# Kernel tuning notes

Measured on AMD Instinct MI355X. Metric: run time of the kernel, lower is better.

The kernel has to match this reference:

```python
import jax, jax.numpy as jnp
import numpy as np

N = 20000      # nodes
E = 80000      # edges (before self loops)
NG = 64        # graphs in batch
EMB = 780      # embedding_size (768 text + 12 time)
NEG_SLOPE = 0.2
BN_EPS = 1e-5


def setup_inputs() -> dict:
    key = jax.random.key(0)
    ks = jax.random.split(key, 20)
    def rn(k, shape, s=0.05):
        return jax.random.normal(k, shape, dtype=jnp.float32) * s
    z = lambda n: jnp.zeros((n,), dtype=jnp.float32)
    o = lambda n: jnp.ones((n,), dtype=jnp.float32)
    x = jax.random.normal(ks[0], (N, 772), dtype=jnp.float32)
    edge_index = jax.random.randint(ks[1], (2, E), 0, N)
    batch = jnp.sort(jax.random.randint(ks[2], (N,), 0, NG))
    return dict(
        x=x, edge_index=edge_index, batch=batch,
        time_W=rn(ks[3], (4, 12)), time_b=z(12),
        lin_W0=rn(ks[4], (EMB, 3 * EMB)), att_src0=rn(ks[5], (3, EMB)), att_dst0=rn(ks[6], (3, EMB)),
        bias0=z(3 * EMB), gamma0=o(3 * EMB), beta0=z(3 * EMB),
        lin_W1=rn(ks[7], (3 * EMB, 3 * EMB)), att_src1=rn(ks[8], (3, EMB)), att_dst1=rn(ks[9], (3, EMB)),
        bias1=z(3 * EMB), gamma1=o(3 * EMB), beta1=z(3 * EMB),
        lin_W2=rn(ks[10], (3 * EMB, EMB)), att_src2=rn(ks[11], (1, EMB)), att_dst2=rn(ks[12], (1, EMB)),
        bias2=z(EMB), gamma2=o(EMB), beta2=z(EMB),
        mlp_W1=rn(ks[13], (EMB, 128)), mlp_b1=z(128),
        mlp_W2=rn(ks[14], (128, 64)), mlp_b2=z(64),
    )


def _gat_layer(h, src, dst, W, a_src, a_dst, b, heads):
    # PyG GATConv (eval mode: dropout off), concat=True, self loops already in src/dst
    C = W.shape[1] // heads
    hp = (h @ W).reshape(N, heads, C)                       # [N,H,C]
    a_s = jnp.sum(hp * a_src[None], axis=-1)                # [N,H]
    a_d = jnp.sum(hp * a_dst[None], axis=-1)                # [N,H]
    e = jax.nn.leaky_relu(a_s[src] + a_d[dst], NEG_SLOPE)   # [E+N,H]
    m = jax.ops.segment_max(e, dst, num_segments=N)         # segment softmax over incoming edges
    m = jnp.where(jnp.isfinite(m), m, 0.0)
    p = jnp.exp(e - m[dst])
    denom = jax.ops.segment_sum(p, dst, num_segments=N)
    alpha = p / (denom[dst] + 1e-16)                        # [E+N,H]
    out = jax.ops.segment_sum(alpha[:, :, None] * hp[src], dst, num_segments=N)  # [N,H,C]
    return out.reshape(N, heads * C) + b


def _bn(h, gamma, beta):
    # BatchNorm in training-mode math (batch statistics, biased variance)
    mu = jnp.mean(h, axis=0)
    var = jnp.mean((h - mu) ** 2, axis=0)
    return (h - mu) * jax.lax.rsqrt(var + BN_EPS) * gamma + beta


def reference(x, edge_index, batch, time_W, time_b,
              lin_W0, att_src0, att_dst0, bias0, gamma0, beta0,
              lin_W1, att_src1, att_dst1, bias1, gamma1, beta1,
              lin_W2, att_src2, att_dst2, bias2, gamma2, beta2,
              mlp_W1, mlp_b1, mlp_W2, mlp_b2):
    te = x[:, 768:772] @ time_W + time_b
    h = jnp.concatenate([jax.lax.stop_gradient(x[:, :768]), te,
                         jax.lax.stop_gradient(x[:, 772:])], axis=-1)  # [N, 780]
    sl = jnp.arange(N)
    src = jnp.concatenate([edge_index[0], sl])   # add self loops
    dst = jnp.concatenate([edge_index[1], sl])
    layers = [
        (lin_W0, att_src0, att_dst0, bias0, gamma0, beta0, 3),
        (lin_W1, att_src1, att_dst1, bias1, gamma1, beta1, 3),
        (lin_W2, att_src2, att_dst2, bias2, gamma2, beta2, 1),
    ]
    for W, a_s, a_d, b, g, bt, heads in layers:
        h = jnp.tanh(_gat_layer(h, src, dst, W, a_s, a_d, b, heads))
        h = _bn(h, g, bt)
    cnt = jax.ops.segment_sum(jnp.ones((N,), dtype=h.dtype), batch, num_segments=NG)
    pooled = jax.ops.segment_sum(h, batch, num_segments=NG) / jnp.maximum(cnt, 1.0)[:, None]
    pooled = jax.nn.relu(pooled)
    out = jnp.tanh(pooled @ mlp_W1 + mlp_b1) @ mlp_W2 + mlp_b2
    return out  # [NG, 64]
```

## Files before the change

kernel.cpp:

```cpp
#include <hip/hip_runtime.h>
#include <math.h>

#define NN   20000
#define EE   80000
#define ELP  100000
#define NGR  64
#define EMB  780
#define W3   2340
#define EMBP 832
#define W3P  2368
#define NZ   (W3+8)

static inline int cdiv_i(long long a, long long b){ return (int)((a + b - 1) / b); }

typedef _Float16 f16;
typedef _Float16 f16x4 __attribute__((ext_vector_type(4)));
typedef _Float16 f16x8 __attribute__((ext_vector_type(8)));
typedef float    f32x4 __attribute__((ext_vector_type(4)));

__device__ __forceinline__ void async_ld16(const f16* g, f16* l){
    __builtin_amdgcn_global_load_lds(
        (const __attribute__((address_space(1))) unsigned int*)g,
        (__attribute__((address_space(3))) unsigned int*)l,
        16, 0, 0);
}

__global__ void k_zero_f32(float* p, int n){
    int i = blockIdx.x*256 + threadIdx.x; if (i < n) p[i] = 0.f;
}
__global__ void k_zero_i32(int* p, int n){
    int i = blockIdx.x*256 + threadIdx.x; if (i < n) p[i] = 0;
}

__global__ void k_transpose(const float* __restrict__ W, f16* __restrict__ Wt,
                            const float* __restrict__ sc, const float* __restrict__ sh,
                            float* __restrict__ dvec, int K, int N, int KP){
    __shared__ float T[32][33];
    __shared__ float D[8][33];
    int n0 = blockIdx.x*32, k0 = blockIdx.y*32;
    int tx = threadIdx.x, ty = threadIdx.y;
    float raw[4];
#pragma unroll
    for (int r = 0; r < 4; r++){
        int k = k0 + ty + r*8;
        float w = 0.f;
        if (k < K && n0 + tx < N) w = W[(size_t)k*N + n0 + tx];
        raw[r] = w;
        T[ty + r*8][tx] = sc ? w * ((k < K) ? sc[k] : 0.f) : w;
    }
    if (sh){
        float p = 0.f;
#pragma unroll
        for (int r = 0; r < 4; r++){
            int k = k0 + ty + r*8;
            if (k < K) p += sh[k] * raw[r];
        }
        D[ty][tx] = p;
    }
    __syncthreads();
#pragma unroll
    for (int r = 0; r < 4; r++){
        int n = n0 + ty + r*8;
        int k = k0 + tx;
        if (n < N && k < KP) Wt[(size_t)n*KP + k] = (f16)T[tx][ty + r*8];
    }
    if (sh && ty == 0 && n0 + tx < N){
        float s = 0.f;
#pragma unroll
        for (int j = 0; j < 8; j++) s += D[j][tx];
        atomicAdd(&dvec[n0 + tx], s);
    }
}

__global__ void k_wvec(const float* __restrict__ W, const float* __restrict__ asrc,
                       const float* __restrict__ adst, const float* __restrict__ sc,
                       f16* __restrict__ Wt, float* __restrict__ dvec,
                       int K, int N, int KP, int H){
    int k = blockIdx.x*4 + (threadIdx.x >> 6);
    int lane = threadIdx.x & 63;
    if (k < K){
        const float* row = W + (size_t)k*N;
        float acc[6];
#pragma unroll
        for (int i = 0; i < 6; i++) acc[i] = 0.f;
        for (int c = lane; c < EMB; c += 64){
            for (int h = 0; h < H; h++){
                float wv = row[h*EMB + c];
                acc[h]     += wv * asrc[h*EMB + c];
                acc[H + h] += wv * adst[h*EMB + c];
            }
        }
        float s = sc ? sc[k] : 1.f;
        for (int i = 0; i < 2*H; i++){
            float v = acc[i];
#pragma unroll
            for (int off = 32; off; off >>= 1) v += __shfl_xor(v, off);
            if (lane == 0) Wt[(size_t)(N + i)*KP + k] = (f16)(v * s);
        }
    }
    if (blockIdx.x == 0){
        int wv = threadIdx.x >> 6;
        for (int i = wv; i < 2*H; i += 4){
            int h = (i < H) ? i : (i - H);
            const float* att = (i < H) ? (asrc + h*EMB) : (adst + h*EMB);
            float s = 0.f;
            for (int c = lane; c < EMB; c += 64) s += dvec[h*EMB + c] * att[c];
#pragma unroll
            for (int off = 32; off; off >>= 1) s += __shfl_xor(s, off);
            if (lane == 0) dvec[N + i] = s;
        }
    }
}

__global__ void k_build_h(const float* __restrict__ x, const float* __restrict__ tW,
                          const float* __restrict__ tb, f16* __restrict__ h){
    int idx = blockIdx.x*256 + threadIdx.x;
    int total = NN*(EMBP/4);
    if (idx >= total) return;
    int n = idx / (EMBP/4);
    int c0 = (idx - n*(EMBP/4))*4;
    const float* xr = x + (size_t)n*772;
    f16x4 o;
#pragma unroll
    for (int j = 0; j < 4; j++){
        int c = c0 + j; float v;
        if (c < 768) v = xr[c];
        else if (c < EMB){
            int t = c - 768;
            v = tb[t] + xr[768]*tW[t] + xr[769]*tW[12+t] + xr[770]*tW[24+t] + xr[771]*tW[36+t];
        } else v = 0.f;
        o[j] = (f16)v;
    }
    *(f16x4*)(h + (size_t)n*EMBP + c0) = o;
}

__global__ void k_deg(const int* __restrict__ ei, int* __restrict__ deg){
    int k = blockIdx.x*256 + threadIdx.x; if (k >= ELP) return;
    int d = (k < EE) ? ei[EE + k] : (k - EE);
    atomicAdd(&deg[d], 1);
}

__global__ __launch_bounds__(1024) void k_scan(int* __restrict__ deg, int* __restrict__ rp){
    __shared__ int part[1024];
    int tid = threadIdx.x;
    int i0 = tid*20;
    int n = (i0 < NN) ? min(20, NN - i0) : 0;
    int s = 0;
    for (int k = 0; k < n; k++) s += deg[i0+k];
    part[tid] = s; __syncthreads();
    for (int off = 1; off < 1024; off <<= 1){
        int t = (tid >= off) ? part[tid-off] : 0;
        __syncthreads();
        part[tid] += t;
        __syncthreads();
    }
    int run = part[tid] - s;
    for (int k = 0; k < n; k++){
        int d = deg[i0+k];
        rp[i0+k] = run;
        deg[i0+k] = run;
        run += d;
    }
    if (tid == 1023) rp[NN] = part[1023];
}

__global__ void k_fill(const int* __restrict__ ei, int* __restrict__ cursor, int* __restrict__ csrc){
    int k = blockIdx.x*256 + threadIdx.x; if (k >= ELP) return;
    int s, d;
    if (k < EE){ s = ei[k]; d = ei[EE + k]; } else { s = k - EE; d = s; }
    int pos = atomicAdd(&cursor[d], 1);
    csrc[pos] = s;
}

__global__ void k_grp(const int* __restrict__ batch, int* __restrict__ grp){
    int g = blockIdx.x*256 + threadIdx.x; if (g > NGR) return;
    int lo = 0, hi = NN;
    while (lo < hi){ int mid = (lo+hi)>>1; if (batch[mid] < g) lo = mid+1; else hi = mid; }
    grp[g] = lo;
}

__global__ __launch_bounds__(256) void k_gemm_mfma(const f16* __restrict__ A,
                                                   const f16* __restrict__ Bt,
                                                   const float* __restrict__ dvec,
                                                   f16* __restrict__ C,
                                                   float* __restrict__ a_sd,
                                                   int M, int N, int NB, int H,
                                                   int KP, int SN,
                                                   int Mtiles, int NT){
    int bid = blockIdx.x;
    int xcd = bid & 7;
    int j   = bid >> 3;
    int sl  = j / NT;
    int nt  = j - sl*NT;
    int mt  = sl*8 + xcd;
    if (mt >= Mtiles) return;
    int m0 = mt*128, n0 = nt*128;

    __shared__ f16 smem[128*136];
    f16* As = smem;
    f16* Bs = smem + 8192;
    int tid = threadIdx.x;
    int w = tid >> 6, lane = tid & 63;

    int lrow = lane >> 2;
    int lko  = (lane & 3) * 8;

    int i2a = w*2, i2b = w*2 + 1;
    const f16* gA0 = A  + (size_t)min(m0 + i2a*16 + lrow, M-1)*KP + lko;
    const f16* gA1 = A  + (size_t)min(m0 + i2b*16 + lrow, M-1)*KP + lko;
    const f16* gB0 = Bt + (size_t)min(n0 + i2a*16 + lrow, NB-1)*KP + lko;
    const f16* gB1 = Bt + (size_t)min(n0 + i2b*16 + lrow, NB-1)*KP + lko;
    f16* lA0 = &As[i2a*512]; f16* lA1 = &As[i2b*512];
    f16* lB0 = &Bs[i2a*512]; f16* lB1 = &Bs[i2b*512];

    f32x4 acc[4][4];
#pragma unroll
    for (int i = 0; i < 4; i++)
#pragma unroll
        for (int j2 = 0; j2 < 4; j2++) acc[i][j2] = (f32x4)0.f;

    int wm = (w & 1) * 64, wn = (w >> 1) * 64;
    int lq = lane >> 4, lm = lane & 15;

    for (int kk = 0; kk < KP; kk += 64){
        __syncthreads();
        async_ld16(gA0 + kk, lA0);
        async_ld16(gA1 + kk, lA1);
        async_ld16(gB0 + kk, lB0);
        async_ld16(gB1 + kk, lB1);
        async_ld16(gA0 + kk + 32, lA0 + 4096);
        async_ld16(gA1 + kk + 32, lA1 + 4096);
        async_ld16(gB0 + kk + 32, lB0 + 4096);
        async_ld16(gB1 + kk + 32, lB1 + 4096);
        __syncthreads();

#pragma unroll
        for (int half = 0; half < 2; half++){
            const f16* Ap = As + half*4096;
            const f16* Bp = Bs + half*4096;
            f16x8 aF[4], bF[4];
#pragma unroll
            for (int mi = 0; mi < 4; mi++)
                aF[mi] = *(const f16x8*)&Ap[(wm + mi*16 + lm)*32 + lq*8];
#pragma unroll
            for (int ni = 0; ni < 4; ni++)
                bF[ni] = *(const f16x8*)&Bp[(wn + ni*16 + lm)*32 + lq*8];
#pragma unroll
            for (int mi = 0; mi < 4; mi++)
#pragma unroll
                for (int ni = 0; ni < 4; ni++)
                    acc[mi][ni] = __builtin_amdgcn_mfma_f32_16x16x32_f16(aF[mi], bF[ni], acc[mi][ni], 0, 0, 0);
        }
    }

#pragma unroll
    for (int mi = 0; mi < 4; mi++){
#pragma unroll
        for (int ni = 0; ni < 4; ni++){
            int col = n0 + wn + ni*16 + lm;
            if (col >= N && col < NB){
                int jc = col - N;
                int idx = (jc < H) ? jc : (3 + jc - H);
                float dv = dvec[col];
                int rbase = m0 + wm + mi*16 + lq*4;
#pragma unroll
                for (int r = 0; r < 4; r++){
                    int row = rbase + r;
                    if (row < M) a_sd[(size_t)row*6 + idx] = acc[mi][ni][r] + dv;
                }
            }
        }
    }

    if (n0 < N){
        __syncthreads();
#pragma unroll
        for (int mi = 0; mi < 4; mi++){
#pragma unroll
            for (int ni = 0; ni < 4; ni++){
                int col = wn + ni*16 + lm;
                int gcol = n0 + col;
                float dv = (gcol < N) ? dvec[gcol] : 0.f;
#pragma unroll
                for (int r = 0; r < 4; r++){
                    int row = wm + mi*16 + lq*4 + r;
                    smem[row*136 + col] = (f16)(acc[mi][ni][r] + dv);
                }
            }
        }
        __syncthreads();
        int ncols = min(128, N - n0);
#pragma unroll
        for (int it = 0; it < 8; it++){
            int ch = tid + it*256;
            int row = ch >> 4, cc = (ch & 15)*8;
            int grow = m0 + row;
            if (grow < M && cc < ncols){
                if (cc + 8 <= ncols){
                    f16x8 v = *(f16x8*)&smem[row*136 + cc];
                    *(f16x8*)(C + (size_t)grow*SN + n0 + cc) = v;
                } else {
                    for (int jj = cc; jj < ncols; jj++)
                        C[(size_t)grow*SN + n0 + jj] = smem[row*136 + jj];
                }
            }
        }
    }
}

template<int H>
__global__ __launch_bounds__(256) void k_agg2(const f16* __restrict__ hp, const int* __restrict__ rp,
                                              const int* __restrict__ csrc, const float* __restrict__ a_sd,
                                              const float* __restrict__ bias,
                                              f16* __restrict__ y, int SP, int W){
    int n = blockIdx.x, tid = threadIdx.x, lane = tid & 63;
    int beg = rp[n], deg = rp[n+1] - beg;

    float adv[H];
#pragma unroll
    for (int h = 0; h < H; h++) adv[h] = a_sd[(size_t)n*6 + 3 + h];

    float mx[H];
#pragma unroll
    for (int h = 0; h < H; h++) mx[h] = -1e30f;
    for (int base = 0; base < deg; base += 64){
        int e = base + lane;
        if (e < deg){
            int s = csrc[beg + e];
#pragma unroll
            for (int h = 0; h < H; h++){
                float t = a_sd[(size_t)s*6 + h] + adv[h];
                t = t > 0.f ? t : 0.2f*t;
                mx[h] = fmaxf(mx[h], t);
            }
        }
    }
#pragma unroll
    for (int off = 32; off; off >>= 1)
#pragma unroll
        for (int h = 0; h < H; h++) mx[h] = fmaxf(mx[h], __shfl_xor(mx[h], off));

    float dn[H];
#pragma unroll
    for (int h = 0; h < H; h++) dn[h] = 0.f;
    for (int base = 0; base < deg; base += 64){
        int e = base + lane;
        if (e < deg){
            int s = csrc[beg + e];
#pragma unroll
            for (int h = 0; h < H; h++){
                float t = a_sd[(size_t)s*6 + h] + adv[h];
                t = t > 0.f ? t : 0.2f*t;
                dn[h] += expf(t - mx[h]);
            }
        }
    }
#pragma unroll
    for (int off = 32; off; off >>= 1)
#pragma unroll
        for (int h = 0; h < H; h++) dn[h] += __shfl_xor(dn[h], off);
    float inv[H];
#pragma unroll
    for (int h = 0; h < H; h++) inv[h] = 1.f / (dn[h] + 1e-16f);

    float acc[2][8];
#pragma unroll
    for (int g = 0; g < 2; g++)
#pragma unroll
        for (int j = 0; j < 8; j++) acc[g][j] = 0.f;
    int  cg[2];  cg[0] = tid*8; cg[1] = 2048 + tid*8;
    bool act[2]; act[0] = cg[0] < W; act[1] = cg[1] < W;
    int hlo[2], hhi[2], nsp[2];
#pragma unroll
    for (int g = 0; g < 2; g++){
        int c = cg[g];
        int hl = min(c / EMB, H-1);
        int hh = min((c+7) / EMB, H-1);
        hlo[g] = hl; hhi[g] = hh;
        nsp[g] = (hh > hl) ? (EMB*(hl+1) - c) : 8;
    }

    for (int base = 0; base < deg; base += 64){
        int cnt = min(64, deg - base);
        int sl = 0; float al[H];
        {
            int e = base + lane;
            if (e < deg){
                sl = csrc[beg + e];
#pragma unroll
                for (int h = 0; h < H; h++){
                    float t = a_sd[(size_t)sl*6 + h] + adv[h];
                    t = t > 0.f ? t : 0.2f*t;
                    al[h] = expf(t - mx[h]) * inv[h];
                }
            } else {
#pragma unroll
                for (int h = 0; h < H; h++) al[h] = 0.f;
            }
        }
#pragma unroll 4
        for (int e = 0; e < cnt; e++){
            int s = __shfl(sl, e);
            float a0 = __shfl(al[0], e);
            float a1 = (H==3) ? __shfl(al[1], e) : a0;
            float a2 = (H==3) ? __shfl(al[2], e) : a0;
            const f16* row = hp + (size_t)s*SP;
#pragma unroll
            for (int g = 0; g < 2; g++){
                if (act[g]){
                    f16x8 v = *(const f16x8*)(row + cg[g]);
                    float lo = (hlo[g]==0) ? a0 : (hlo[g]==1 ? a1 : a2);
                    float hi = (hhi[g]==0) ? a0 : (hhi[g]==1 ? a1 : a2);
#pragma unroll
                    for (int j = 0; j < 8; j++){
                        float alj = (j < nsp[g]) ? lo : hi;
                        acc[g][j] += alj * (float)v[j];
                    }
                }
            }
        }
    }

#pragma unroll
    for (int g = 0; g < 2; g++){
        int c = cg[g];
        if (c < SP){
            f16x8 o;
#pragma unroll
            for (int j = 0; j < 8; j++){
                float vv = (c + j < W) ? tanhf(acc[g][j] + bias[c+j]) : 0.f;
                o[j] = (f16)vv;
            }
            *(f16x8*)(y + (size_t)n*SP + c) = o;
        }
    }
}

__global__ void k_bnstat(const f16* __restrict__ y, float* __restrict__ ps,
                         float* __restrict__ pq, int W, int SP){
    int c0 = (blockIdx.x*256 + threadIdx.x)*4;
    if (c0 >= W) return;
    int slice = blockIdx.y;
    int r0 = (int)(((long long)NN*slice)/128);
    int r1 = (int)(((long long)NN*(slice+1))/128);
    float s[4] = {0,0,0,0}, q[4] = {0,0,0,0};
    for (int r = r0; r < r1; r++){
        f16x4 u = *(const f16x4*)(y + (size_t)r*SP + c0);
#pragma unroll
        for (int j = 0; j < 4; j++){ float v = (float)u[j]; s[j] += v; q[j] += v*v; }
    }
#pragma unroll
    for (int j = 0; j < 4; j++){
        ps[(size_t)slice*W3 + c0+j] = s[j];
        pq[(size_t)slice*W3 + c0+j] = q[j];
    }
}

__global__ void k_bnfin(const float* __restrict__ ps, const float* __restrict__ pq,
                        const float* __restrict__ gamma, const float* __restrict__ beta,
                        float* __restrict__ sc, float* __restrict__ sh,
                        float* __restrict__ dvec, int W, int zn){
    int c = blockIdx.x*256 + threadIdx.x;
    if (c < W){
        float m = 0.f, q = 0.f;
        for (int s = 0; s < 128; s++){ m += ps[(size_t)s*W3 + c]; q += pq[(size_t)s*W3 + c]; }
        m *= (1.f/NN);
        float v = q * (1.f/NN) - m*m;
        float is = 1.f / sqrtf(v + 1e-5f);
        float g = gamma[c];
        sc[c] = is * g;
        sh[c] = beta[c] - m * is * g;
    }
    if (c < zn) dvec[c] = 0.f;
}

__global__ void k_pool(const f16* __restrict__ h, const int* __restrict__ grp,
                       float* __restrict__ pooled){
    int g = blockIdx.x;
    int c = threadIdx.x*4;
    if (c >= EMB) return;
    int r0 = grp[g], r1 = grp[g+1];
    float s0=0.f, s1=0.f, s2=0.f, s3=0.f;
    for (int r = r0; r < r1; r++){
        f16x4 u = *(const f16x4*)(h + (size_t)r*EMBP + c);
        s0 += (float)u[0]; s1 += (float)u[1]; s2 += (float)u[2]; s3 += (float)u[3];
    }
    pooled[g*EMB + c] = s0; pooled[g*EMB + c+1] = s1;
    pooled[g*EMB + c+2] = s2; pooled[g*EMB + c+3] = s3;
}

__global__ __launch_bounds__(256) void k_mlp(const float* __restrict__ pooled, const int* __restrict__ grp,
                                             const float* __restrict__ sc, const float* __restrict__ sh,
                                             const float* __restrict__ W1, const float* __restrict__ b1,
                                             const float* __restrict__ W2, const float* __restrict__ b2,
                                             float* __restrict__ out){
    __shared__ float p[EMB];
    __shared__ float hid[128];
    int g = blockIdx.x, tid = threadIdx.x;
    int cnt = grp[g+1] - grp[g];
    float ic = 1.f / fmaxf((float)cnt, 1.f);
    for (int c = tid; c < EMB; c += 256){
        float v = pooled[g*EMB + c] * ic * sc[c] + sh[c];
        p[c] = v > 0.f ? v : 0.f;
    }
    __syncthreads();
    if (tid < 128){
        float s = b1[tid];
        for (int k = 0; k < EMB; k++) s += p[k] * W1[k*128 + tid];
        hid[tid] = tanhf(s);
    }
    __syncthreads();
    if (tid < 64){
        float s = b2[tid];
        for (int k = 0; k < 128; k++) s += hid[k] * W2[k*64 + tid];
        out[g*64 + tid] = s;
    }
}

extern "C" void kernel_launch(void* const* d_in, const int* in_sizes, int n_in,
                              void* d_out, int out_size, void* d_ws, size_t ws_size,
                              hipStream_t stream) {
    (void)in_sizes; (void)n_in; (void)out_size;
    const float* x    = (const float*)d_in[0];
    const int*   ei   = (const int*)  d_in[1];
    const int*   batch= (const int*)  d_in[2];
    const float* tW   = (const float*)d_in[3];
    const float* tb   = (const float*)d_in[4];
    const float* W0   = (const float*)d_in[5];
    const float* as0  = (const float*)d_in[6];
    const float* ad0  = (const float*)d_in[7];
    const float* b0   = (const float*)d_in[8];
    const float* g0   = (const float*)d_in[9];
    const float* be0  = (const float*)d_in[10];
    const float* W1   = (const float*)d_in[11];
    const float* as1  = (const float*)d_in[12];
    const float* ad1  = (const float*)d_in[13];
    const float* b1   = (const float*)d_in[14];
    const float* g1   = (const float*)d_in[15];
    const float* be1  = (const float*)d_in[16];
    const float* W2   = (const float*)d_in[17];
    const float* as2  = (const float*)d_in[18];
    const float* ad2  = (const float*)d_in[19];
    const float* b2   = (const float*)d_in[20];
    const float* g2   = (const float*)d_in[21];
    const float* be2  = (const float*)d_in[22];
    const float* mW1  = (const float*)d_in[23];
    const float* mb1  = (const float*)d_in[24];
    const float* mW2  = (const float*)d_in[25];
    const float* mb2  = (const float*)d_in[26];
    float* outp = (float*)d_out;

    size_t off = 0;
    auto carve = [&](size_t bytes) -> void* {
        void* p = (char*)d_ws + off;
        off = (off + bytes + 255) & ~(size_t)255;
        return p;
    };
    f16* big1 = (f16*)carve((size_t)NN*W3P*2);
    f16* big2 = (f16*)carve((size_t)NN*W3P*2);
    f16* Wt   = (f16*)carve((size_t)NZ*W3P*2);
    float* a_sd  = (float*)carve((size_t)NN*6*4);
    float* psum  = (float*)carve((size_t)128*W3*4);
    float* psq   = (float*)carve((size_t)128*W3*4);
    float* sc    = (float*)carve((size_t)W3*4);
    float* sh    = (float*)carve((size_t)W3*4);
    float* dvec  = (float*)carve((size_t)NZ*4);
    float* pooled= (float*)carve((size_t)NGR*EMB*4);
    int*   grp   = (int*)carve((size_t)(NGR+1)*4);
    int*   deg   = (int*)carve((size_t)NN*4);
    int*   rp    = (int*)carve((size_t)(NN+1)*4);
    int*   csrc  = (int*)carve((size_t)ELP*4);

    if (ws_size < off) return;

    k_zero_i32<<<cdiv_i(NN,256),256,0,stream>>>(deg, NN);
    k_deg<<<cdiv_i(ELP,256),256,0,stream>>>(ei, deg);
    k_scan<<<1,1024,0,stream>>>(deg, rp);
    k_fill<<<cdiv_i(ELP,256),256,0,stream>>>(ei, deg, csrc);
    k_grp<<<1,256,0,stream>>>(batch, grp);

    k_build_h<<<cdiv_i((long long)NN*(EMBP/4),256),256,0,stream>>>(x, tW, tb, big1);
    k_zero_f32<<<cdiv_i(NZ,256),256,0,stream>>>(dvec, NZ);

    struct Layer { const float* W; const float* as; const float* ad; const float* b;
                   const float* g; const float* be; int H; int K; int KP; };
    Layer layers[3] = {
        {W0, as0, ad0, b0, g0, be0, 3, EMB, EMBP},
        {W1, as1, ad1, b1, g1, be1, 3, W3,  W3P },
        {W2, as2, ad2, b2, g2, be2, 1, W3,  W3P },
    };

    for (int L = 0; L < 3; L++){
        Layer& ly = layers[L];
        int Wout  = ly.H * EMB;
        int NB    = Wout + 2*ly.H;
        int SPout = (Wout == W3) ? W3P : EMBP;
        const float* scale = (L == 0) ? nullptr : sc;
        const float* shift = (L == 0) ? nullptr : sh;

        dim3 tg(cdiv_i(Wout,32), cdiv_i(ly.KP,32));
        k_transpose<<<tg, dim3(32,8), 0, stream>>>(ly.W, Wt, scale, shift, dvec, ly.K, Wout, ly.KP);
        k_wvec<<<cdiv_i(ly.K,4),256,0,stream>>>(ly.W, ly.as, ly.ad, scale, Wt, dvec, ly.K, Wout, ly.KP, ly.H);

        int Mtiles = cdiv_i(NN,128), NT = cdiv_i(NB,128);
        int nb = ((Mtiles+7)/8)*8*NT;
        k_gemm_mfma<<<nb, 256, 0, stream>>>(big1, Wt, dvec, big2, a_sd,
                                            NN, Wout, NB, ly.H, ly.KP, SPout, Mtiles, NT);

        if (ly.H == 3)
            k_agg2<3><<<NN,256,0,stream>>>(big2, rp, csrc, a_sd, ly.b, big1, SPout, Wout);
        else
            k_agg2<1><<<NN,256,0,stream>>>(big2, rp, csrc, a_sd, ly.b, big1, SPout, Wout);

        dim3 gs(cdiv_i(Wout/4,256), 128);
        k_bnstat<<<gs,256,0,stream>>>(big1, psum, psq, Wout, SPout);
        int zn = (L < 2) ? NZ : 0;
        k_bnfin<<<cdiv_i(Wout,256),256,0,stream>>>(psum, psq, ly.g, ly.be, sc, sh, dvec, Wout, zn);
    }

    k_pool<<<NGR,256,0,stream>>>(big1, grp, pooled);
    k_mlp<<<NGR,256,0,stream>>>(pooled, grp, sc, sh, mW1, mb1, mW2, mb2, outp);
}
```

Measured before the change: 1.478 ms.

## Replace GEMM with 256x256 tile, 8-wave, double-buffered pipelined MFMA kernel

Replaces the 128x128 single-buffered MFMA GEMM with a 256x256 tile kernel using 512 threads and 8 waves. It double-buffers the K slices in LDS with async global-to-LDS loads issued between MFMA clusters, XOR-swizzles the LDS layout to avoid bank conflicts, and raises MFMA priority with setprio. Workgroups are remapped so consecutive tiles land on the same XCD. The aim is to hide load latency and raise data reuse. The cost is fewer workgroups, more padding waste at tile edges, and fragile hand-written waitcnt and barrier choreography.

```diff
diff --git a/kernel.cpp b/kernel.cpp
--- a/kernel.cpp
+++ b/kernel.cpp
@@ -179,129 +179,188 @@
     grp[g] = lo;
 }
 
-__global__ __launch_bounds__(256) void k_gemm_mfma(const f16* __restrict__ A,
-                                                   const f16* __restrict__ Bt,
-                                                   const float* __restrict__ dvec,
-                                                   f16* __restrict__ C,
-                                                   float* __restrict__ a_sd,
-                                                   int M, int N, int NB, int H,
-                                                   int KP, int SN,
-                                                   int Mtiles, int NT){
+__global__ __launch_bounds__(512, 2) void k_gemm8(const f16* __restrict__ A,
+                                                  const f16* __restrict__ Bt,
+                                                  const float* __restrict__ dvec,
+                                                  f16* __restrict__ C,
+                                                  float* __restrict__ a_sd,
+                                                  int M, int N, int NB, int H,
+                                                  int KP, int SN, int Mtiles, int NT){
+    __shared__ f16 sA[65536];
+    f16* sB = sA + 32768;
+
+    int nwg = Mtiles*NT;
     int bid = blockIdx.x;
-    int xcd = bid & 7;
-    int j   = bid >> 3;
-    int sl  = j / NT;
-    int nt  = j - sl*NT;
-    int mt  = sl*8 + xcd;
-    if (mt >= Mtiles) return;
-    int m0 = mt*128, n0 = nt*128;
-
-    __shared__ f16 smem[128*136];
-    f16* As = smem;
-    f16* Bs = smem + 8192;
+    int q = nwg >> 3, r = nwg & 7, xcd = bid & 7, lin = bid >> 3;
+    int wg = (xcd < r ? xcd*(q+1) : r*(q+1) + (xcd - r)*q) + lin;
+    int mt = wg / NT, nt = wg - mt*NT;
+    int m0 = mt*256, n0 = nt*256;
+
     int tid = threadIdx.x;
     int w = tid >> 6, lane = tid & 63;
-
-    int lrow = lane >> 2;
-    int lko  = (lane & 3) * 8;
-
-    int i2a = w*2, i2b = w*2 + 1;
-    const f16* gA0 = A  + (size_t)min(m0 + i2a*16 + lrow, M-1)*KP + lko;
-    const f16* gA1 = A  + (size_t)min(m0 + i2b*16 + lrow, M-1)*KP + lko;
-    const f16* gB0 = Bt + (size_t)min(n0 + i2a*16 + lrow, NB-1)*KP + lko;
-    const f16* gB1 = Bt + (size_t)min(n0 + i2b*16 + lrow, NB-1)*KP + lko;
-    f16* lA0 = &As[i2a*512]; f16* lA1 = &As[i2b*512];
-    f16* lB0 = &Bs[i2a*512]; f16* lB1 = &Bs[i2b*512];
-
-    f32x4 acc[4][4];
-#pragma unroll
-    for (int i = 0; i < 4; i++)
-#pragma unroll
-        for (int j2 = 0; j2 < 4; j2++) acc[i][j2] = (f32x4)0.f;
-
-    int wm = (w & 1) * 64, wn = (w >> 1) * 64;
-    int lq = lane >> 4, lm = lane & 15;
-
-    for (int kk = 0; kk < KP; kk += 64){
-        __syncthreads();
-        async_ld16(gA0 + kk, lA0);
-        async_ld16(gA1 + kk, lA1);
-        async_ld16(gB0 + kk, lB0);
-        async_ld16(gB1 + kk, lB1);
-        async_ld16(gA0 + kk + 32, lA0 + 4096);
-        async_ld16(gA1 + kk + 32, lA1 + 4096);
-        async_ld16(gB0 + kk + 32, lB0 + 4096);
-        async_ld16(gB1 + kk + 32, lB1 + 4096);
-        __syncthreads();
-
-#pragma unroll
-        for (int half = 0; half < 2; half++){
-            const f16* Ap = As + half*4096;
-            const f16* Bp = Bs + half*4096;
-            f16x8 aF[4], bF[4];
-#pragma unroll
-            for (int mi = 0; mi < 4; mi++)
-                aF[mi] = *(const f16x8*)&Ap[(wm + mi*16 + lm)*32 + lq*8];
-#pragma unroll
-            for (int ni = 0; ni < 4; ni++)
-                bF[ni] = *(const f16x8*)&Bp[(wn + ni*16 + lm)*32 + lq*8];
-#pragma unroll
-            for (int mi = 0; mi < 4; mi++)
-#pragma unroll
-                for (int ni = 0; ni < 4; ni++)
-                    acc[mi][ni] = __builtin_amdgcn_mfma_f32_16x16x32_f16(aF[mi], bF[ni], acc[mi][ni], 0, 0, 0);
-        }
-    }
-
-#pragma unroll
-    for (int mi = 0; mi < 4; mi++){
+    int lm = lane & 15, lq = lane >> 4;
+    int wm = w >> 2, wn = w & 3;
+
+    int rstage0 = w*32 + (lane >> 2);
+    int rstage1 = rstage0 + 16;
+    int kqs = ((lane & 3) ^ ((lane >> 3) & 3)) * 8;
+    const f16* gA0 = A  + (size_t)min(m0 + rstage0, M-1)*KP + kqs;
+    const f16* gA1 = A  + (size_t)min(m0 + rstage1, M-1)*KP + kqs;
+    const f16* gB0 = Bt + (size_t)min(n0 + rstage0, NB-1)*KP + kqs;
+    const f16* gB1 = Bt + (size_t)min(n0 + rstage1, NB-1)*KP + kqs;
+    int so0 = w*1024, so1 = w*1024 + 512;
+
+    int swz  = (lq ^ ((lm >> 1) & 3)) * 8;
+    int aoff = (wm*128 + lm)*32 + swz;
+    int boff = (wn*64  + lm)*32 + swz;
+
+    f32x4 acc[8][4];
+#pragma unroll
+    for (int i = 0; i < 8; i++)
+#pragma unroll
+        for (int j = 0; j < 4; j++) acc[i][j] = (f32x4)0.f;
+
+    int KT = KP >> 6;
+
+    async_ld16(gA0,      &sA[so0]);         async_ld16(gA1,      &sA[so1]);
+    async_ld16(gB0,      &sB[so0]);         async_ld16(gB1,      &sB[so1]);
+    async_ld16(gA0 + 32, &sA[8192+so0]);    async_ld16(gA1 + 32, &sA[8192+so1]);
+    async_ld16(gB0 + 32, &sB[8192+so0]);    async_ld16(gB1 + 32, &sB[8192+so1]);
+    async_ld16(gA0 + 64, &sA[16384+so0]);   async_ld16(gA1 + 64, &sA[16384+so1]);
+    async_ld16(gB0 + 64, &sB[16384+so0]);   async_ld16(gB1 + 64, &sB[16384+so1]);
+    asm volatile("s_waitcnt vmcnt(4)" ::: "memory");
+    __builtin_amdgcn_s_barrier();
+
+    for (int t = 0; t < KT; t++){
+        int buf  = (t & 1) << 14;
+        int nbuf = buf ^ 16384;
+        bool s1 = (t+1 < KT), s2 = (t+2 < KT);
+        int ko1 = (t+1)*64, ko2 = (t+2)*64;
+        f16x8 aF[4], bF[4];
+
+#pragma unroll
+        for (int i = 0; i < 4; i++) aF[i] = *(const f16x8*)&sA[buf + aoff + i*512];
+#pragma unroll
+        for (int i = 0; i < 4; i++) bF[i] = *(const f16x8*)&sB[buf + boff + i*512];
+        if (s1){ async_ld16(gA0+ko1+32, &sA[nbuf+8192+so0]); async_ld16(gA1+ko1+32, &sA[nbuf+8192+so1]); }
+        __builtin_amdgcn_s_barrier();
+        asm volatile("s_waitcnt lgkmcnt(0)" ::: "memory");
+        __builtin_amdgcn_sched_barrier(0);
+        __builtin_amdgcn_s_setprio(1);
+#pragma unroll
+        for (int i = 0; i < 4; i++)
+#pragma unroll
+            for (int j = 0; j < 4; j++)
+                acc[i][j] = __builtin_amdgcn_mfma_f32_16x16x32_f16(aF[i], bF[j], acc[i][j], 0, 0, 0);
+        __builtin_amdgcn_s_setprio(0);
+        __builtin_amdgcn_s_barrier();
+
+#pragma unroll
+        for (int i = 0; i < 4; i++) aF[i] = *(const f16x8*)&sA[buf + aoff + 2048 + i*512];
+        if (s1){ async_ld16(gB0+ko1+32, &sB[nbuf+8192+so0]); async_ld16(gB1+ko1+32, &sB[nbuf+8192+so1]); }
+        __builtin_amdgcn_s_barrier();
+        asm volatile("s_waitcnt lgkmcnt(0)" ::: "memory");
+        __builtin_amdgcn_sched_barrier(0);
+        __builtin_amdgcn_s_setprio(1);
+#pragma unroll
+        for (int i = 0; i < 4; i++)
+#pragma unroll
+            for (int j = 0; j < 4; j++)
+                acc[4+i][j] = __builtin_amdgcn_mfma_f32_16x16x32_f16(aF[i], bF[j], acc[4+i][j], 0, 0, 0);
+        __builtin_amdgcn_s_setprio(0);
+        __builtin_amdgcn_s_barrier();
+
+#pragma unroll
+        for (int i = 0; i < 4; i++) aF[i] = *(const f16x8*)&sA[buf + 8192 + aoff + i*512];
+#pragma unroll
+        for (int i = 0; i < 4; i++) bF[i] = *(const f16x8*)&sB[buf + 8192 + boff + i*512];
+        if (s2){ async_ld16(gA0+ko2, &sA[buf+so0]); async_ld16(gA1+ko2, &sA[buf+so1]); }
+        __builtin_amdgcn_s_barrier();
+        asm volatile("s_waitcnt lgkmcnt(0)" ::: "memory");
+        __builtin_amdgcn_sched_barrier(0);
+        __builtin_amdgcn_s_setprio(1);
+#pragma unroll
+        for (int i = 0; i < 4; i++)
+#pragma unroll
+            for (int j = 0; j < 4; j++)
+                acc[i][j] = __builtin_amdgcn_mfma_f32_16x16x32_f16(aF[i], bF[j], acc[i][j], 0, 0, 0);
+        __builtin_amdgcn_s_setprio(0);
+        __builtin_amdgcn_s_barrier();
+
+#pragma unroll
+        for (int i = 0; i < 4; i++) aF[i] = *(const f16x8*)&sA[buf + 8192 + aoff + 2048 + i*512];
+        if (s2){ async_ld16(gB0+ko2, &sB[buf+so0]); async_ld16(gB1+ko2, &sB[buf+so1]); }
+        __builtin_amdgcn_s_barrier();
+        asm volatile("s_waitcnt lgkmcnt(0)" ::: "memory");
+        __builtin_amdgcn_sched_barrier(0);
+        __builtin_amdgcn_s_setprio(1);
+#pragma unroll
+        for (int i = 0; i < 4; i++)
+#pragma unroll
+            for (int j = 0; j < 4; j++)
+                acc[4+i][j] = __builtin_amdgcn_mfma_f32_16x16x32_f16(aF[i], bF[j], acc[4+i][j], 0, 0, 0);
+        __builtin_amdgcn_s_setprio(0);
+        if (s2) asm volatile("s_waitcnt vmcnt(4)" ::: "memory");
+        else    asm volatile("s_waitcnt vmcnt(0)" ::: "memory");
+        __builtin_amdgcn_s_barrier();
+    }
+
+#pragma unroll
+    for (int mi = 0; mi < 8; mi++){
 #pragma unroll
         for (int ni = 0; ni < 4; ni++){
-            int col = n0 + wn + ni*16 + lm;
+            int col = n0 + wn*64 + ni*16 + lm;
             if (col >= N && col < NB){
                 int jc = col - N;
                 int idx = (jc < H) ? jc : (3 + jc - H);
                 float dv = dvec[col];
-                int rbase = m0 + wm + mi*16 + lq*4;
-#pragma unroll
-                for (int r = 0; r < 4; r++){
-                    int row = rbase + r;
-                    if (row < M) a_sd[(size_t)row*6 + idx] = acc[mi][ni][r] + dv;
+                int rbase = m0 + wm*128 + mi*16 + lq*4;
+#pragma unroll
+                for (int rr = 0; rr < 4; rr++){
+                    int row = rbase + rr;
+                    if (row < M) a_sd[(size_t)row*6 + idx] = acc[mi][ni][rr] + dv;
                 }
             }
         }
     }
 
-    if (n0 < N){
-        __syncthreads();
-#pragma unroll
-        for (int mi = 0; mi < 4; mi++){
-#pragma unroll
-            for (int ni = 0; ni < 4; ni++){
-                int col = wn + ni*16 + lm;
-                int gcol = n0 + col;
-                float dv = (gcol < N) ? dvec[gcol] : 0.f;
-#pragma unroll
-                for (int r = 0; r < 4; r++){
-                    int row = wm + mi*16 + lq*4 + r;
-                    smem[row*136 + col] = (f16)(acc[mi][ni][r] + dv);
+    float dv4[4];
+#pragma unroll
+    for (int ni = 0; ni < 4; ni++){
+        int gcol = n0 + wn*64 + ni*16 + lm;
+        dv4[ni] = (gcol < N) ? dvec[gcol] : 0.f;
+    }
+    int ncols = min(256, N - n0);
+#pragma unroll
+    for (int hh = 0; hh < 2; hh++){
+        __builtin_amdgcn_s_barrier();
+        if (wm == hh){
+#pragma unroll
+            for (int mi = 0; mi < 8; mi++){
+#pragma unroll
+                for (int ni = 0; ni < 4; ni++){
+                    int colL = wn*64 + ni*16 + lm;
+#pragma unroll
+                    for (int rr = 0; rr < 4; rr++){
+                        int rowL = mi*16 + lq*4 + rr;
+                        sA[rowL*264 + colL] = (f16)(acc[mi][ni][rr] + dv4[ni]);
+                    }
                 }
             }
         }
-        __syncthreads();
-        int ncols = min(128, N - n0);
+        __builtin_amdgcn_s_barrier();
 #pragma unroll
         for (int it = 0; it < 8; it++){
-            int ch = tid + it*256;
-            int row = ch >> 4, cc = (ch & 15)*8;
-            int grow = m0 + row;
+            int ch = tid + it*512;
+            int rowL = ch >> 5, cc = (ch & 31)*8;
+            int grow = m0 + hh*128 + rowL;
             if (grow < M && cc < ncols){
                 if (cc + 8 <= ncols){
-                    f16x8 v = *(f16x8*)&smem[row*136 + cc];
+                    f16x8 v = *(f16x8*)&sA[rowL*264 + cc];
                     *(f16x8*)(C + (size_t)grow*SN + n0 + cc) = v;
                 } else {
                     for (int jj = cc; jj < ncols; jj++)
-                        C[(size_t)grow*SN + n0 + jj] = smem[row*136 + jj];
+                        C[(size_t)grow*SN + n0 + jj] = sA[rowL*264 + jj];
                 }
             }
         }
@@ -602,10 +661,9 @@
         k_transpose<<<tg, dim3(32,8), 0, stream>>>(ly.W, Wt, scale, shift, dvec, ly.K, Wout, ly.KP);
         k_wvec<<<cdiv_i(ly.K,4),256,0,stream>>>(ly.W, ly.as, ly.ad, scale, Wt, dvec, ly.K, Wout, ly.KP, ly.H);
 
-        int Mtiles = cdiv_i(NN,128), NT = cdiv_i(NB,128);
-        int nb = ((Mtiles+7)/8)*8*NT;
-        k_gemm_mfma<<<nb, 256, 0, stream>>>(big1, Wt, dvec, big2, a_sd,
-                                            NN, Wout, NB, ly.H, ly.KP, SPout, Mtiles, NT);
+        int Mtiles = cdiv_i(NN,256), NT = cdiv_i(NB,256);
+        k_gemm8<<<Mtiles*NT, 512, 0, stream>>>(big1, Wt, dvec, big2, a_sd,
+                                               NN, Wout, NB, ly.H, ly.KP, SPout, Mtiles, NT);
 
         if (ly.H == 3)
             k_agg2<3><<<NN,256,0,stream>>>(big2, rp, csrc, a_sd, ly.b, big1, SPout, Wout);
```

Measured after the change: 1.521 ms. 2.9% more time.
